# Optimization experiments

Hardware: AMD Instinct MI355X
Metric: run time of the kernel (lower is better)

## Reference

```python
import jax, jax.numpy as jnp
import numpy as np

B, N, IN_DIM, D, H, L = 8, 256, 2, 128, 512, 2
EPS = 1e-5


def layer_norm(x, g, b):
    m = jnp.mean(x, axis=-1, keepdims=True)
    v = jnp.var(x, axis=-1, keepdims=True)
    return (x - m) * jax.lax.rsqrt(v + EPS) * g + b


def loo_max_pool(nodes):
    # nodes: (B, N, D) -> leave-one-out max over the set axis -> (B, N, D)
    n = nodes.shape[1]
    neg = jnp.finfo(nodes.dtype).min
    mask = jnp.eye(n, dtype=bool)[None, :, :, None]          # (1, N, N, 1)
    expanded = jnp.broadcast_to(nodes[:, None, :, :],
                                (nodes.shape[0], n, n, nodes.shape[2]))
    return jnp.where(mask, neg, expanded).max(axis=2)        # (B, N, D)


def setup_inputs() -> dict:
    key = jax.random.key(0)
    ks = jax.random.split(key, 16)
    s = 0.02
    inp = {
        "x":   jax.random.normal(ks[0], (B, N, IN_DIM), dtype=jnp.float32),
        # embedding linear + its LayerNorm
        "We":  jax.random.normal(ks[1], (IN_DIM, D)) * s,
        "be":  jnp.zeros((D,), jnp.float32),
        "ge":  jnp.ones((D,), jnp.float32),
        "bge": jnp.zeros((D,), jnp.float32),
        # per-layer pool linear (concat of x and LOO-pooled context: 2D -> D)
        "Wp":  jax.random.normal(ks[2], (L, 2 * D, D)) * s,
        "bp":  jnp.zeros((L, D), jnp.float32),
        "gp":  jnp.ones((L, D), jnp.float32),
        "bgp": jnp.zeros((L, D), jnp.float32),
        # per-layer feed-forward D -> H -> D
        "W1":  jax.random.normal(ks[3], (L, D, H)) * s,
        "b1":  jnp.zeros((L, H), jnp.float32),
        "W2":  jax.random.normal(ks[4], (L, H, D)) * s,
        "b2":  jnp.zeros((L, D), jnp.float32),
        "gf":  jnp.ones((L, D), jnp.float32),
        "bgf": jnp.zeros((L, D), jnp.float32),
    }
    return inp


def reference(x, We, be, ge, bge, Wp, bp, gp, bgp, W1, b1, W2, b2, gf, bgf):
    # embeddings + embedding norm
    h = layer_norm(x @ We + be, ge, bge)                      # (B, N, D)
    for i in range(L):
        # pool layer: LOO max pooling, concat, linear, residual, norm
        pooled = loo_max_pool(h)                              # (B, N, D)
        cat = jnp.concatenate([h, pooled], axis=-1)           # (B, N, 2D)
        h = layer_norm(h + cat @ Wp[i] + bp[i], gp[i], bgp[i])
        # feed-forward, residual, norm
        ff = jax.nn.relu(h @ W1[i] + b1[i]) @ W2[i] + b2[i]
        h = layer_norm(h + ff, gf[i], bgf[i])
    return h
```

## Files before the change

kernel.cpp:

```cpp
#include <hip/hip_runtime.h>
#include <hip/hip_bf16.h>

#define BB 8
#define NN 256
#define DD 128
#define HH 512
#define LL 2
#define EPSV 1e-5f
#define TPE 4
#define TPB 8
#define BPE (NN/TPE)
#define BPL (NN/TPB)

typedef unsigned short ushort_t;
typedef __attribute__((ext_vector_type(8))) short bf16x8;
typedef __attribute__((ext_vector_type(4))) float f32x4;

__device__ __forceinline__ ushort_t f2b(float v){
  __hip_bfloat16 h = __float2bfloat16(v);
  return *(ushort_t*)&h;
}

__device__ __forceinline__ void waveRed2(float &a, float &b){
  #pragma unroll
  for (int off=32; off>=1; off>>=1){
    a += __shfl_xor(a, off, 64);
    b += __shfl_xor(b, off, 64);
  }
}

__device__ __forceinline__ void poolMerge(float &m1, float &m2, int &am,
                                          float o1, float o2, int oa){
  if (o1 > m1){ m2 = fmaxf(m1, o2); m1 = o1; am = oa; }
  else        { m2 = fmaxf(m2, o1); }
}

__global__ __launch_bounds__(256) void k_conv(
    const float* __restrict__ Wp, const float* __restrict__ W1,
    const float* __restrict__ W2, ushort_t* __restrict__ wpT,
    ushort_t* __restrict__ w1T, ushort_t* __restrict__ w2T)
{
  __shared__ float tile[32][33];
  int bid = blockIdx.x;
  const float* src; ushort_t* dst; int K, N, kt, nt;
  if (bid < 64){
    int l = bid >> 5, r = bid & 31;
    src = Wp + (size_t)l*256*128; dst = wpT + (size_t)l*128*256;
    K=256; N=128; kt = r >> 2; nt = r & 3;
  } else if (bid < 192){
    int e = bid - 64; int l = e >> 6, r = e & 63;
    src = W1 + (size_t)l*128*512; dst = w1T + (size_t)l*512*128;
    K=128; N=512; kt = r >> 4; nt = r & 15;
  } else {
    int e = bid - 192; int l = e >> 6, r = e & 63;
    src = W2 + (size_t)l*512*128; dst = w2T + (size_t)l*128*512;
    K=512; N=128; kt = r >> 2; nt = r & 3;
  }
  int k0 = kt*32, n0 = nt*32;
  int tx = threadIdx.x & 31, ty = threadIdx.x >> 5;
  #pragma unroll
  for (int i=0;i<4;++i)
    tile[ty + i*8][tx] = src[(size_t)(k0+ty+i*8)*N + n0 + tx];
  __syncthreads();
  #pragma unroll
  for (int i=0;i<4;++i)
    dst[(size_t)(n0+ty+i*8)*K + k0 + tx] = f2b(tile[tx][ty + i*8]);
}

__global__ __launch_bounds__(512) void k_embed(
    const float* __restrict__ x, const float* __restrict__ We,
    const float* __restrict__ be, const float* __restrict__ ge,
    const float* __restrict__ bge, float* __restrict__ h,
    float* __restrict__ pm1p, float* __restrict__ pm2p, int* __restrict__ pargp)
{
  int tid = threadIdx.x;
  int t = tid >> 7, d = tid & 127;
  int lane = tid & 63, wid = (tid >> 6) & 1;
  int t0 = blockIdx.x * TPE;
  int tok = t0 + t;
  __shared__ float red[TPE][2][2];
  __shared__ float hf[TPE][DD];
  float x0 = x[tok*2], x1 = x[tok*2+1];
  float v = fmaf(x0, We[d], fmaf(x1, We[DD+d], be[d]));
  float s=v, q=v*v; waveRed2(s,q);
  if (lane==0){ red[t][wid][0]=s; red[t][wid][1]=q; }
  __syncthreads();
  float S=red[t][0][0]+red[t][1][0], Q=red[t][0][1]+red[t][1][1];
  float m=S*(1.f/DD), var=Q*(1.f/DD)-m*m, rs=rsqrtf(var+EPSV);
  float hv = (v-m)*rs*ge[d] + bge[d];
  h[(size_t)tok*DD + d] = hv;
  hf[t][d] = hv;
  __syncthreads();
  if (t==0){
    int b = t0 >> 8;
    int n0 = t0 & 255;
    float m1 = hf[0][d], m2 = -3.4e38f; int am = n0;
    #pragma unroll
    for (int p=1;p<TPE;++p) poolMerge(m1,m2,am, hf[p][d], -3.4e38f, n0+p);
    int blk = (t0 >> 2) & (BPE-1);
    size_t idx = ((size_t)b*BPE + blk)*DD + d;
    pm1p[idx]=m1; pm2p[idx]=m2; pargp[idx]=am;
  }
}

__global__ __launch_bounds__(512) void k_layer(
    float* __restrict__ h,
    const float* __restrict__ pm1p, const float* __restrict__ pm2p,
    const int* __restrict__ pargp, int npart,
    float* __restrict__ qm1p, float* __restrict__ qm2p, int* __restrict__ qargp,
    int write_pool,
    const ushort_t* __restrict__ WpT, const float* __restrict__ bp,
    const float* __restrict__ gp, const float* __restrict__ bgp,
    const ushort_t* __restrict__ W1T, const float* __restrict__ b1,
    const ushort_t* __restrict__ W2T, const float* __restrict__ b2,
    const float* __restrict__ gf, const float* __restrict__ bgf)
{
  int tid = threadIdx.x;
  int d = tid & 127, fourth = tid >> 7;
  int wv = tid >> 6;
  int lane = tid & 63;
  int m = lane & 15, q = lane >> 4;
  int t0 = blockIdx.x * TPB;
  int b = t0 >> 8;

  __shared__ ushort_t catb[16*256];
  __shared__ float    hres[8*128];
  __shared__ float    sA[16*128];
  __shared__ ushort_t h1b[16*128];
  __shared__ float    h1f[8*128];
  __shared__ ushort_t ub[16*512];
  __shared__ float fm1[128], fm2[128];
  __shared__ int   fam[128];
  __shared__ float sm1[4][128], sm2[4][128];
  __shared__ int   sam[4][128];

  {
    int per = npart >> 2;
    size_t base = ((size_t)b*npart + fourth*per)*DD + d;
    float m1 = pm1p[base], m2 = pm2p[base]; int am = pargp[base];
    for (int i=1;i<per;++i)
      poolMerge(m1,m2,am, pm1p[base+(size_t)i*DD], pm2p[base+(size_t)i*DD],
                pargp[base+(size_t)i*DD]);
    sm1[fourth][d]=m1; sm2[fourth][d]=m2; sam[fourth][d]=am;
  }
  __syncthreads();
  if (fourth==0){
    float m1=sm1[0][d], m2=sm2[0][d]; int am=sam[0][d];
    #pragma unroll
    for (int p=1;p<4;++p) poolMerge(m1,m2,am, sm1[p][d], sm2[p][d], sam[p][d]);
    fm1[d]=m1; fm2[d]=m2; fam[d]=am;
  }
  __syncthreads();

  #pragma unroll
  for (int rep=0; rep<4; ++rep){
    int e = rep*512 + tid;
    int t = e >> 8, c = e & 255;
    int tok = t0 + t, n = (t0 & 255) + t;
    float v;
    if (c < DD){ v = h[(size_t)tok*DD + c]; hres[t*128 + c] = v; }
    else { int cc = c - DD; v = (n==fam[cc]) ? fm2[cc] : fm1[cc]; }
    catb[t*256 + c] = f2b(v);
  }
  __syncthreads();

  {
    int n0 = wv*16;
    f32x4 acc = {0.f,0.f,0.f,0.f};
    const ushort_t* ap = catb + m*256 + q*8;
    const ushort_t* wp = WpT + (size_t)(n0+m)*256 + q*8;
    #pragma unroll
    for (int ks=0; ks<8; ++ks){
      bf16x8 af = *(const bf16x8*)(ap + ks*32);
      bf16x8 wf = *(const bf16x8*)(wp + ks*32);
      acc = __builtin_amdgcn_mfma_f32_16x16x32_bf16(af, wf, acc, 0,0,0);
    }
    #pragma unroll
    for (int r=0;r<4;++r) sA[(q*4+r)*128 + n0 + m] = acc[r];
  }
  __syncthreads();

  {
    int t = wv, g = lane;
    float2 v2 = *(const float2*)&sA[t*128 + 2*g];
    float v0 = v2.x + bp[2*g]   + hres[t*128 + 2*g];
    float v1 = v2.y + bp[2*g+1] + hres[t*128 + 2*g + 1];
    float s = v0+v1, qq = v0*v0 + v1*v1;
    waveRed2(s,qq);
    float mean = s*(1.f/128), var = qq*(1.f/128) - mean*mean;
    float rs = rsqrtf(var + EPSV);
    float o0 = (v0-mean)*rs*gp[2*g]   + bgp[2*g];
    float o1 = (v1-mean)*rs*gp[2*g+1] + bgp[2*g+1];
    unsigned pk = (unsigned)f2b(o0) | ((unsigned)f2b(o1) << 16);
    *(unsigned*)&h1b[t*128 + 2*g] = pk;
    *(float2*)&h1f[t*128 + 2*g] = make_float2(o0, o1);
  }
  __syncthreads();

  {
    const ushort_t* ap = h1b + m*128 + q*8;
    #pragma unroll
    for (int i=0;i<4;++i){
      int n0 = i*128 + wv*16;
      f32x4 acc = {0.f,0.f,0.f,0.f};
      const ushort_t* wp = W1T + (size_t)(n0+m)*128 + q*8;
      #pragma unroll
      for (int ks=0; ks<4; ++ks){
        bf16x8 af = *(const bf16x8*)(ap + ks*32);
        bf16x8 wf = *(const bf16x8*)(wp + ks*32);
        acc = __builtin_amdgcn_mfma_f32_16x16x32_bf16(af, wf, acc, 0,0,0);
      }
      float bb = b1[n0+m];
      #pragma unroll
      for (int r=0;r<4;++r)
        ub[(q*4+r)*512 + n0 + m] = f2b(fmaxf(acc[r] + bb, 0.f));
    }
  }
  __syncthreads();

  {
    int n0 = wv*16;
    f32x4 acc = {0.f,0.f,0.f,0.f};
    const ushort_t* ap = ub + m*512 + q*8;
    const ushort_t* wp = W2T + (size_t)(n0+m)*512 + q*8;
    #pragma unroll
    for (int ks=0; ks<16; ++ks){
      bf16x8 af = *(const bf16x8*)(ap + ks*32);
      bf16x8 wf = *(const bf16x8*)(wp + ks*32);
      acc = __builtin_amdgcn_mfma_f32_16x16x32_bf16(af, wf, acc, 0,0,0);
    }
    #pragma unroll
    for (int r=0;r<4;++r) sA[(q*4+r)*128 + n0 + m] = acc[r];
  }
  __syncthreads();

  {
    int t = wv, g = lane;
    float2 v2 = *(const float2*)&sA[t*128 + 2*g];
    float v0 = v2.x + b2[2*g]   + h1f[t*128 + 2*g];
    float v1 = v2.y + b2[2*g+1] + h1f[t*128 + 2*g + 1];
    float s = v0+v1, qq = v0*v0 + v1*v1;
    waveRed2(s,qq);
    float mean = s*(1.f/128), var = qq*(1.f/128) - mean*mean;
    float rs = rsqrtf(var + EPSV);
    float o0 = (v0-mean)*rs*gf[2*g]   + bgf[2*g];
    float o1 = (v1-mean)*rs*gf[2*g+1] + bgf[2*g+1];
    *(float2*)&h[(size_t)(t0+t)*DD + 2*g] = make_float2(o0, o1);
    *(float2*)&hres[t*128 + 2*g] = make_float2(o0, o1);
  }
  if (write_pool){
    __syncthreads();
    if (tid < 128){
      int n0 = t0 & 255;
      float m1 = hres[tid], m2 = -3.4e38f; int am = n0;
      #pragma unroll
      for (int p=1;p<TPB;++p)
        poolMerge(m1,m2,am, hres[p*128 + tid], -3.4e38f, n0+p);
      int blk = (t0 >> 3) & (BPL-1);
      size_t idx = ((size_t)b*BPL + blk)*DD + tid;
      qm1p[idx]=m1; qm2p[idx]=m2; qargp[idx]=am;
    }
  }
}

extern "C" void kernel_launch(void* const* d_in, const int* in_sizes, int n_in,
                              void* d_out, int out_size, void* d_ws, size_t ws_size,
                              hipStream_t stream)
{
  const float* x   = (const float*)d_in[0];
  const float* We  = (const float*)d_in[1];
  const float* be  = (const float*)d_in[2];
  const float* ge  = (const float*)d_in[3];
  const float* bge = (const float*)d_in[4];
  const float* Wp  = (const float*)d_in[5];
  const float* bp  = (const float*)d_in[6];
  const float* gp  = (const float*)d_in[7];
  const float* bgp = (const float*)d_in[8];
  const float* W1  = (const float*)d_in[9];
  const float* b1  = (const float*)d_in[10];
  const float* W2  = (const float*)d_in[11];
  const float* b2  = (const float*)d_in[12];
  const float* gf  = (const float*)d_in[13];
  const float* bgf = (const float*)d_in[14];

  float* h = (float*)d_out;
  char* ws = (char*)d_ws;
  const size_t NA = (size_t)BB*BPE*DD;
  const size_t NB = (size_t)BB*BPL*DD;
  float* pA1 = (float*)ws;                    ws += NA*4;
  float* pA2 = (float*)ws;                    ws += NA*4;
  int*   pAa = (int*)ws;                      ws += NA*4;
  float* pB1 = (float*)ws;                    ws += NB*4;
  float* pB2 = (float*)ws;                    ws += NB*4;
  int*   pBa = (int*)ws;                      ws += NB*4;
  ushort_t* wpT = (ushort_t*)ws;              ws += (size_t)LL*DD*2*DD*2;
  ushort_t* w1T = (ushort_t*)ws;              ws += (size_t)LL*HH*DD*2;
  ushort_t* w2T = (ushort_t*)ws;              ws += (size_t)LL*DD*HH*2;

  k_conv<<<320, 256, 0, stream>>>(Wp, W1, W2, wpT, w1T, w2T);

  k_embed<<<(BB*NN)/TPE, 512, 0, stream>>>(x, We, be, ge, bge, h, pA1, pA2, pAa);

  k_layer<<<(BB*NN)/TPB, 512, 0, stream>>>(h, pA1, pA2, pAa, BPE,
      pB1, pB2, pBa, 1,
      wpT,                     bp,       gp,       bgp,
      w1T,                     b1,       w2T,      b2,
      gf,                      bgf);

  k_layer<<<(BB*NN)/TPB, 512, 0, stream>>>(h, pB1, pB2, pBa, BPL,
      pB1, pB2, pBa, 0,
      wpT + (size_t)DD*2*DD,   bp + DD,  gp + DD,  bgp + DD,
      w1T + (size_t)HH*DD,     b1 + HH,  w2T + (size_t)DD*HH, b2 + DD,
      gf + DD,                 bgf + DD);
}
```

Before: 123.2 us.

## Merge embed and weight-convert kernels; prefetch MFMA weights into registers early

Folds the weight transpose/convert kernel and the embedding kernel into one launch, with blocks split by index, which removes one kernel launch and its serialization gap. In the layer kernel, the bf16 weight fragments for all three GEMMs are loaded into registers at the start, or between stages, so their global latency overlaps the pooling reduction and earlier MFMA work. The W1 stage also hoists its A-fragment loads out of the N loop. The cost is much higher register pressure (40 bf16x8 fragments per thread) under launch_bounds(512,2), which may cause spilling or lower occupancy.

```diff
diff --git a/kernel.cpp b/kernel.cpp
--- a/kernel.cpp
+++ b/kernel.cpp
@@ -11,6 +11,7 @@
 #define TPB 8
 #define BPE (NN/TPE)
 #define BPL (NN/TPB)
+#define NEMB ((BB*NN)/TPE)
 
 typedef unsigned short ushort_t;
 typedef __attribute__((ext_vector_type(8))) short bf16x8;
@@ -35,75 +36,76 @@
   else        { m2 = fmaxf(m2, o1); }
 }
 
-__global__ __launch_bounds__(256) void k_conv(
+__global__ __launch_bounds__(512) void k_prep(
+    const float* __restrict__ x, const float* __restrict__ We,
+    const float* __restrict__ be, const float* __restrict__ ge,
+    const float* __restrict__ bge, float* __restrict__ h,
+    float* __restrict__ pm1p, float* __restrict__ pm2p, int* __restrict__ pargp,
     const float* __restrict__ Wp, const float* __restrict__ W1,
     const float* __restrict__ W2, ushort_t* __restrict__ wpT,
     ushort_t* __restrict__ w1T, ushort_t* __restrict__ w2T)
 {
   __shared__ float tile[32][33];
-  int bid = blockIdx.x;
-  const float* src; ushort_t* dst; int K, N, kt, nt;
-  if (bid < 64){
-    int l = bid >> 5, r = bid & 31;
-    src = Wp + (size_t)l*256*128; dst = wpT + (size_t)l*128*256;
-    K=256; N=128; kt = r >> 2; nt = r & 3;
-  } else if (bid < 192){
-    int e = bid - 64; int l = e >> 6, r = e & 63;
-    src = W1 + (size_t)l*128*512; dst = w1T + (size_t)l*512*128;
-    K=128; N=512; kt = r >> 4; nt = r & 15;
-  } else {
-    int e = bid - 192; int l = e >> 6, r = e & 63;
-    src = W2 + (size_t)l*512*128; dst = w2T + (size_t)l*128*512;
-    K=512; N=128; kt = r >> 2; nt = r & 3;
-  }
-  int k0 = kt*32, n0 = nt*32;
-  int tx = threadIdx.x & 31, ty = threadIdx.x >> 5;
-  #pragma unroll
-  for (int i=0;i<4;++i)
-    tile[ty + i*8][tx] = src[(size_t)(k0+ty+i*8)*N + n0 + tx];
-  __syncthreads();
-  #pragma unroll
-  for (int i=0;i<4;++i)
-    dst[(size_t)(n0+ty+i*8)*K + k0 + tx] = f2b(tile[tx][ty + i*8]);
-}
-
-__global__ __launch_bounds__(512) void k_embed(
-    const float* __restrict__ x, const float* __restrict__ We,
-    const float* __restrict__ be, const float* __restrict__ ge,
-    const float* __restrict__ bge, float* __restrict__ h,
-    float* __restrict__ pm1p, float* __restrict__ pm2p, int* __restrict__ pargp)
-{
-  int tid = threadIdx.x;
-  int t = tid >> 7, d = tid & 127;
-  int lane = tid & 63, wid = (tid >> 6) & 1;
-  int t0 = blockIdx.x * TPE;
-  int tok = t0 + t;
   __shared__ float red[TPE][2][2];
   __shared__ float hf[TPE][DD];
-  float x0 = x[tok*2], x1 = x[tok*2+1];
-  float v = fmaf(x0, We[d], fmaf(x1, We[DD+d], be[d]));
-  float s=v, q=v*v; waveRed2(s,q);
-  if (lane==0){ red[t][wid][0]=s; red[t][wid][1]=q; }
-  __syncthreads();
-  float S=red[t][0][0]+red[t][1][0], Q=red[t][0][1]+red[t][1][1];
-  float m=S*(1.f/DD), var=Q*(1.f/DD)-m*m, rs=rsqrtf(var+EPSV);
-  float hv = (v-m)*rs*ge[d] + bge[d];
-  h[(size_t)tok*DD + d] = hv;
-  hf[t][d] = hv;
-  __syncthreads();
-  if (t==0){
-    int b = t0 >> 8;
-    int n0 = t0 & 255;
-    float m1 = hf[0][d], m2 = -3.4e38f; int am = n0;
-    #pragma unroll
-    for (int p=1;p<TPE;++p) poolMerge(m1,m2,am, hf[p][d], -3.4e38f, n0+p);
-    int blk = (t0 >> 2) & (BPE-1);
-    size_t idx = ((size_t)b*BPE + blk)*DD + d;
-    pm1p[idx]=m1; pm2p[idx]=m2; pargp[idx]=am;
-  }
-}
-
-__global__ __launch_bounds__(512) void k_layer(
+
+  if (blockIdx.x < NEMB){
+    int tid = threadIdx.x;
+    int t = tid >> 7, d = tid & 127;
+    int lane = tid & 63, wid = (tid >> 6) & 1;
+    int t0 = blockIdx.x * TPE;
+    int tok = t0 + t;
+    float x0 = x[tok*2], x1 = x[tok*2+1];
+    float v = fmaf(x0, We[d], fmaf(x1, We[DD+d], be[d]));
+    float s=v, q=v*v; waveRed2(s,q);
+    if (lane==0){ red[t][wid][0]=s; red[t][wid][1]=q; }
+    __syncthreads();
+    float S=red[t][0][0]+red[t][1][0], Q=red[t][0][1]+red[t][1][1];
+    float m=S*(1.f/DD), var=Q*(1.f/DD)-m*m, rs=rsqrtf(var+EPSV);
+    float hv = (v-m)*rs*ge[d] + bge[d];
+    h[(size_t)tok*DD + d] = hv;
+    hf[t][d] = hv;
+    __syncthreads();
+    if (t==0){
+      int b = t0 >> 8;
+      int n0 = t0 & 255;
+      float m1 = hf[0][d], m2 = -3.4e38f; int am = n0;
+      #pragma unroll
+      for (int p=1;p<TPE;++p) poolMerge(m1,m2,am, hf[p][d], -3.4e38f, n0+p);
+      int blk = (t0 >> 2) & (BPE-1);
+      size_t idx = ((size_t)b*BPE + blk)*DD + d;
+      pm1p[idx]=m1; pm2p[idx]=m2; pargp[idx]=am;
+    }
+  } else {
+    if (threadIdx.x >= 256) return;
+    int bid = blockIdx.x - NEMB;
+    const float* src; ushort_t* dst; int K, N, kt, nt;
+    if (bid < 64){
+      int l = bid >> 5, r = bid & 31;
+      src = Wp + (size_t)l*256*128; dst = wpT + (size_t)l*128*256;
+      K=256; N=128; kt = r >> 2; nt = r & 3;
+    } else if (bid < 192){
+      int e = bid - 64; int l = e >> 6, r = e & 63;
+      src = W1 + (size_t)l*128*512; dst = w1T + (size_t)l*512*128;
+      K=128; N=512; kt = r >> 4; nt = r & 15;
+    } else {
+      int e = bid - 192; int l = e >> 6, r = e & 63;
+      src = W2 + (size_t)l*512*128; dst = w2T + (size_t)l*128*512;
+      K=512; N=128; kt = r >> 2; nt = r & 3;
+    }
+    int k0 = kt*32, n0 = nt*32;
+    int tx = threadIdx.x & 31, ty = threadIdx.x >> 5;
+    #pragma unroll
+    for (int i=0;i<4;++i)
+      tile[ty + i*8][tx] = src[(size_t)(k0+ty+i*8)*N + n0 + tx];
+    __syncthreads();
+    #pragma unroll
+    for (int i=0;i<4;++i)
+      dst[(size_t)(n0+ty+i*8)*K + k0 + tx] = f2b(tile[tx][ty + i*8]);
+  }
+}
+
+__global__ __launch_bounds__(512, 2) void k_layer(
     float* __restrict__ h,
     const float* __restrict__ pm1p, const float* __restrict__ pm2p,
     const int* __restrict__ pargp, int npart,
@@ -134,6 +136,24 @@
   __shared__ float sm1[4][128], sm2[4][128];
   __shared__ int   sam[4][128];
 
+  int n0a = wv*16;
+  bf16x8 wfA[8];
+  {
+    const ushort_t* wp = WpT + (size_t)(n0a+m)*256 + q*8;
+    #pragma unroll
+    for (int ks=0; ks<8; ++ks) wfA[ks] = *(const bf16x8*)(wp + ks*32);
+  }
+  bf16x8 wfB[16];
+  {
+    #pragma unroll
+    for (int i=0;i<4;++i){
+      int n0 = i*128 + wv*16;
+      const ushort_t* wp = W1T + (size_t)(n0+m)*128 + q*8;
+      #pragma unroll
+      for (int ks=0; ks<4; ++ks) wfB[i*4+ks] = *(const bf16x8*)(wp + ks*32);
+    }
+  }
+
   {
     int per = npart >> 2;
     size_t base = ((size_t)b*npart + fourth*per)*DD + d;
@@ -165,18 +185,22 @@
   __syncthreads();
 
   {
-    int n0 = wv*16;
     f32x4 acc = {0.f,0.f,0.f,0.f};
     const ushort_t* ap = catb + m*256 + q*8;
-    const ushort_t* wp = WpT + (size_t)(n0+m)*256 + q*8;
     #pragma unroll
     for (int ks=0; ks<8; ++ks){
       bf16x8 af = *(const bf16x8*)(ap + ks*32);
-      bf16x8 wf = *(const bf16x8*)(wp + ks*32);
-      acc = __builtin_amdgcn_mfma_f32_16x16x32_bf16(af, wf, acc, 0,0,0);
-    }
-    #pragma unroll
-    for (int r=0;r<4;++r) sA[(q*4+r)*128 + n0 + m] = acc[r];
+      acc = __builtin_amdgcn_mfma_f32_16x16x32_bf16(af, wfA[ks], acc, 0,0,0);
+    }
+    #pragma unroll
+    for (int r=0;r<4;++r) sA[(q*4+r)*128 + n0a + m] = acc[r];
+  }
+
+  bf16x8 wfC[16];
+  {
+    const ushort_t* wp = W2T + (size_t)(n0a+m)*512 + q*8;
+    #pragma unroll
+    for (int ks=0; ks<16; ++ks) wfC[ks] = *(const bf16x8*)(wp + ks*32);
   }
   __syncthreads();
 
@@ -199,17 +223,16 @@
 
   {
     const ushort_t* ap = h1b + m*128 + q*8;
+    bf16x8 af[4];
+    #pragma unroll
+    for (int ks=0; ks<4; ++ks) af[ks] = *(const bf16x8*)(ap + ks*32);
     #pragma unroll
     for (int i=0;i<4;++i){
       int n0 = i*128 + wv*16;
       f32x4 acc = {0.f,0.f,0.f,0.f};
-      const ushort_t* wp = W1T + (size_t)(n0+m)*128 + q*8;
-      #pragma unroll
-      for (int ks=0; ks<4; ++ks){
-        bf16x8 af = *(const bf16x8*)(ap + ks*32);
-        bf16x8 wf = *(const bf16x8*)(wp + ks*32);
-        acc = __builtin_amdgcn_mfma_f32_16x16x32_bf16(af, wf, acc, 0,0,0);
-      }
+      #pragma unroll
+      for (int ks=0; ks<4; ++ks)
+        acc = __builtin_amdgcn_mfma_f32_16x16x32_bf16(af[ks], wfB[i*4+ks], acc, 0,0,0);
       float bb = b1[n0+m];
       #pragma unroll
       for (int r=0;r<4;++r)
@@ -219,18 +242,15 @@
   __syncthreads();
 
   {
-    int n0 = wv*16;
     f32x4 acc = {0.f,0.f,0.f,0.f};
     const ushort_t* ap = ub + m*512 + q*8;
-    const ushort_t* wp = W2T + (size_t)(n0+m)*512 + q*8;
     #pragma unroll
     for (int ks=0; ks<16; ++ks){
       bf16x8 af = *(const bf16x8*)(ap + ks*32);
-      bf16x8 wf = *(const bf16x8*)(wp + ks*32);
-      acc = __builtin_amdgcn_mfma_f32_16x16x32_bf16(af, wf, acc, 0,0,0);
-    }
-    #pragma unroll
-    for (int r=0;r<4;++r) sA[(q*4+r)*128 + n0 + m] = acc[r];
+      acc = __builtin_amdgcn_mfma_f32_16x16x32_bf16(af, wfC[ks], acc, 0,0,0);
+    }
+    #pragma unroll
+    for (int r=0;r<4;++r) sA[(q*4+r)*128 + n0a + m] = acc[r];
   }
   __syncthreads();
 
@@ -297,9 +317,8 @@
   ushort_t* w1T = (ushort_t*)ws;              ws += (size_t)LL*HH*DD*2;
   ushort_t* w2T = (ushort_t*)ws;              ws += (size_t)LL*DD*HH*2;
 
-  k_conv<<<320, 256, 0, stream>>>(Wp, W1, W2, wpT, w1T, w2T);
-
-  k_embed<<<(BB*NN)/TPE, 512, 0, stream>>>(x, We, be, ge, bge, h, pA1, pA2, pAa);
+  k_prep<<<NEMB + 320, 512, 0, stream>>>(x, We, be, ge, bge, h,
+      pA1, pA2, pAa, Wp, W1, W2, wpT, w1T, w2T);
 
   k_layer<<<(BB*NN)/TPB, 512, 0, stream>>>(h, pA1, pA2, pAa, BPE,
       pB1, pB2, pBa, 1,
```

Result: no change. 123.1 us (-0.1%).
